# Optimization experiments

Measured on AMD Instinct MI355X. Metric: run time of the kernel, lower is better.

Reference implementation:

```python
import jax, jax.numpy as jnp
import numpy as np

K = 3
K2 = K * K
STRIDE, PAD, DIL = 1, 1, 1


def conv2d(x, w, b, stride, pad, dil):
    out = jax.lax.conv_general_dilated(
        x, w, (stride, stride), [(pad, pad), (pad, pad)],
        rhs_dilation=(dil, dil),
        dimension_numbers=("NCHW", "OIHW", "NCHW"))
    return out + b[None, :, None, None]


def deform_sample(img, py, px):
    """Bilinear sample with zero padding outside.
    img: [C,H,W]; py,px: [K2,Ho,Wo] float sample coords -> [C,K2,Ho,Wo]."""
    C, H, W = img.shape
    y0 = jnp.floor(py)
    x0 = jnp.floor(px)
    acc = jnp.zeros((C,) + py.shape, img.dtype)
    for dy in (0.0, 1.0):
        for dx in (0.0, 1.0):
            yi = y0 + dy
            xi = x0 + dx
            wgt = (1.0 - jnp.abs(py - yi)) * (1.0 - jnp.abs(px - xi))
            valid = (yi >= 0) & (yi < H) & (xi >= 0) & (xi < W)
            yc = jnp.clip(yi, 0, H - 1).astype(jnp.int32)
            xc = jnp.clip(xi, 0, W - 1).astype(jnp.int32)
            v = img[:, yc, xc]  # gather -> [C,K2,Ho,Wo]
            acc = acc + v * (wgt * valid)[None]
    return acc


def setup_inputs() -> dict:
    key = jax.random.key(0)
    k1, k2, k3, k4 = jax.random.split(key, 4)
    Cin, Cout = 64, 64
    x = jax.random.normal(k1, (4, Cin, 128, 128), jnp.float32)
    # small offset-conv weights so learned offsets stay in a few-pixel range
    w_off = jax.random.normal(k2, (3 * K2, Cin, K, K), jnp.float32) * 0.01
    b_off = jnp.zeros((3 * K2,), jnp.float32)
    # folded (BN-fused) deform conv weight/bias
    w = jax.random.normal(k3, (Cout, Cin, K, K), jnp.float32) * (1.0 / np.sqrt(Cin * K2))
    b = jax.random.normal(k4, (Cout,), jnp.float32) * 0.1
    return {"x": x, "w_off": w_off, "b_off": b_off, "w": w, "b": b}


def reference(x, w_off, b_off, w, b):
    N, C, H, W = x.shape
    # offset/mask conv -> chunk into (o1, o2, mask), cat offsets, sigmoid mask
    om = conv2d(x, w_off, b_off, STRIDE, PAD, DIL)  # [N, 27, Ho, Wo]
    o1, o2, m = jnp.split(om, 3, axis=1)
    offset = jnp.concatenate([o1, o2], axis=1)      # [N, 2*K2, Ho, Wo]
    mask = jax.nn.sigmoid(m)                        # [N, K2, Ho, Wo]
    Ho, Wo = offset.shape[2], offset.shape[3]
    # torchvision layout: per kernel tap (dy, dx) pairs
    off = offset.reshape(N, K2, 2, Ho, Wo)
    dy, dx = off[:, :, 0], off[:, :, 1]
    hk, wk = jnp.meshgrid(jnp.arange(K), jnp.arange(K), indexing="ij")
    base_y = ((jnp.arange(Ho) * STRIDE - PAD)[None, :, None]
              + (hk.reshape(K2) * DIL)[:, None, None])  # [K2,Ho,1]
    base_x = ((jnp.arange(Wo) * STRIDE - PAD)[None, None, :]
              + (wk.reshape(K2) * DIL)[:, None, None])  # [K2,1,Wo]
    py = base_y.astype(x.dtype) + dy                    # [N,K2,Ho,Wo]
    px = base_x.astype(x.dtype) + dx
    sampled = jax.vmap(deform_sample)(x, py, px)        # [N,C,K2,Ho,Wo]
    sampled = sampled * mask[:, None]
    out = jnp.einsum("ock,nckhw->nohw", w.reshape(w.shape[0], C, K2), sampled)
    out = out + b[None, :, None, None]
    return jax.nn.relu(out)
```

## Files before the change

kernel.cpp:

```cpp
#include <hip/hip_runtime.h>
#include <math.h>

#define N_ 4
#define C_ 64
#define H_ 128
#define W_ 128
#define HW_ (H_ * W_)
#define K2_ 9
#define COUT 64
#define CK 576
#define TP 16
#define SST 584

typedef __bf16 bf16x8 __attribute__((ext_vector_type(8)));
typedef __bf16 bf16x2 __attribute__((ext_vector_type(2)));
typedef float floatx4 __attribute__((ext_vector_type(4)));
typedef float floatx2 __attribute__((ext_vector_type(2)));

__device__ __forceinline__ float bflo(unsigned u) {
    return __builtin_bit_cast(float, u << 16);
}
__device__ __forceinline__ float bfhi(unsigned u) {
    return __builtin_bit_cast(float, u & 0xffff0000u);
}

__global__ __launch_bounds__(256) void prep_kernel(const float* __restrict__ x,
                                                   const float* __restrict__ w,
                                                   const float* __restrict__ w_off,
                                                   __bf16* __restrict__ xT,
                                                   __bf16* __restrict__ w2,
                                                   __bf16* __restrict__ w_off2) {
    __shared__ float s_t[64][33];
    int t = threadIdx.x;
    int bx = blockIdx.x;
    int y = blockIdx.y, n = blockIdx.z;
    if (bx < 4) {
        int x0 = bx * 32;
        int c = t >> 2, seg = (t & 3) * 8;
        const float* src = x + (((size_t)n * C_ + c) * H_ + y) * W_ + x0 + seg;
        floatx4 v0 = *(const floatx4*)src;
        floatx4 v1 = *(const floatx4*)(src + 4);
#pragma unroll
        for (int j = 0; j < 4; ++j) { s_t[c][seg + j] = v0[j]; s_t[c][seg + 4 + j] = v1[j]; }
        __syncthreads();
        int xl = t >> 3, cb = (t & 7) * 8;
        bf16x8 o;
#pragma unroll
        for (int j = 0; j < 8; ++j) o[j] = (__bf16)s_t[cb + j][xl];
        *(bf16x8*)(xT + (((size_t)n * H_ + y) * W_ + x0 + xl) * C_ + cb) = o;
    } else {
        int linear = (n * 128 + y) * 256 + t;
        if (linear < COUT * CK) {
            int o = linear / CK, r = linear - o * CK;
            int k = r >> 6, c = r & 63;
            w2[linear] = (__bf16)w[(o * C_ + c) * K2_ + k];
        }
        if (linear < 32 * CK) {
            int o = linear / CK, r = linear - o * CK;
            int k = r >> 6, c = r & 63;
            w_off2[linear] = (o < 27) ? (__bf16)w_off[(o * C_ + c) * K2_ + k] : (__bf16)0.f;
        }
    }
}

__device__ __forceinline__ floatx4 gemm_tile(const __bf16* __restrict__ arow,
                                             const __bf16* __restrict__ brow) {
    floatx4 acc = {0.f, 0.f, 0.f, 0.f};
#pragma unroll
    for (int it = 0; it < 18; ++it) {
        bf16x8 a  = *(const bf16x8*)(arow + 32 * it);
        bf16x8 bb = *(const bf16x8*)(brow + 32 * it);
        acc = __builtin_amdgcn_mfma_f32_16x16x32_bf16(a, bb, acc, 0, 0, 0);
    }
    return acc;
}

__global__ __launch_bounds__(256) void fused_kernel(const __bf16* __restrict__ xT,
                                                    const __bf16* __restrict__ w2,
                                                    const __bf16* __restrict__ w_off2,
                                                    const float* __restrict__ b_off,
                                                    const float* __restrict__ b,
                                                    float* __restrict__ out) {
    __shared__ __align__(16) __bf16 s_x[TP * SST];
    __shared__ float s_om[32 * TP];
    __shared__ floatx4 s_w4[K2_ * TP];
    __shared__ int s_pix[K2_ * TP];

    int t = threadIdx.x;
    int pixbase = blockIdx.x * TP;
    int wo0 = pixbase & (W_ - 1);
    int ho  = (pixbase >> 7) & (H_ - 1);
    int n   = pixbase >> 14;
    const __bf16* xn = xT + (size_t)n * HW_ * C_;

    int lane = t & 63;
    int wv   = t >> 6;
    int half = lane >> 5;
    int li   = lane & 31;

    {
        unsigned ua[18];
#pragma unroll
        for (int j = 0; j < 18; ++j) {
            int P = wv * 36 + 2 * j + half;
            int k = P >> 4, p = P & 15;
            int kh = k / 3, kw = k - kh * 3;
            int y  = ho - 1 + kh;
            int xx = wo0 + p - 1 + kw;
            int yc  = min(max(y, 0), H_ - 1);
            int xc2 = min(max(xx, 0), W_ - 1);
            unsigned pix = (unsigned)(yc * W_ + xc2);
            ua[j] = *(const unsigned*)(xn + (size_t)pix * C_ + 2 * li);
        }
#pragma unroll
        for (int j = 0; j < 18; ++j) {
            int P = wv * 36 + 2 * j + half;
            int k = P >> 4, p = P & 15;
            int kh = k / 3, kw = k - kh * 3;
            int y  = ho - 1 + kh;
            int xx = wo0 + p - 1 + kw;
            bool valid = ((unsigned)y < (unsigned)H_) && ((unsigned)xx < (unsigned)W_);
            unsigned v = valid ? ua[j] : 0u;
            *(unsigned*)&s_x[p * SST + k * 64 + 2 * li] = v;
        }
    }
    __syncthreads();

    int q   = lane >> 4;
    int col = lane & 15;
    const __bf16* brow = s_x + col * SST + q * 8;

    if (wv < 2) {
        int row = min(16 * wv + col, 26);
        floatx4 acc = gemm_tile(w_off2 + (size_t)row * CK + q * 8, brow);
#pragma unroll
        for (int r = 0; r < 4; ++r)
            s_om[(16 * wv + q * 4 + r) * TP + col] = acc[r];
    }
    __syncthreads();

    if (t < K2_ * TP) {
        int k  = t >> 4;
        int pp = t & 15;
        float dy = s_om[(2 * k) * TP + pp]     + b_off[2 * k];
        float dx = s_om[(2 * k + 1) * TP + pp] + b_off[2 * k + 1];
        float mm = s_om[(18 + k) * TP + pp]    + b_off[18 + k];
        float msk = 1.f / (1.f + expf(-mm));
        int kh = k / 3, kw = k - kh * 3;
        float py = (float)(ho - 1 + kh) + dy;
        float px = (float)(wo0 + pp - 1 + kw) + dx;
        float yf = floorf(py), xf = floorf(px);
        float fy = py - yf, fx = px - xf;
        int y0 = (int)yf, x0 = (int)xf;
        float wy0 = ((unsigned)y0 < (unsigned)H_)       ? 1.f - fy : 0.f;
        float wy1 = ((unsigned)(y0 + 1) < (unsigned)H_) ? fy       : 0.f;
        float wx0 = ((unsigned)x0 < (unsigned)W_)       ? 1.f - fx : 0.f;
        float wx1 = ((unsigned)(x0 + 1) < (unsigned)W_) ? fx       : 0.f;
        int y0c = min(max(y0, 0), H_ - 2);
        int x0c = min(max(x0, 0), W_ - 2);
        float t0 = (y0 == y0c) ? wy0 : ((y0 + 1 == y0c) ? wy1 : 0.f);
        float t1 = (y0 == y0c) ? wy1 : ((y0 == y0c + 1) ? wy0 : 0.f);
        float u0 = (x0 == x0c) ? wx0 : ((x0 + 1 == x0c) ? wx1 : 0.f);
        float u1 = (x0 == x0c) ? wx1 : ((x0 == x0c + 1) ? wx0 : 0.f);
        floatx4 w4 = { t0 * u0 * msk, t0 * u1 * msk, t1 * u0 * msk, t1 * u1 * msk };
        s_w4[t] = w4;
        s_pix[t] = y0c * W_ + x0c;
    }
    __syncthreads();

    {
        int Pb = wv * 36 + half;
        unsigned buf[3][4];
#pragma unroll
        for (int g = 0; g < 2; ++g) {
            int pix = s_pix[Pb + 2 * g];
            const unsigned* bp = (const unsigned*)(xn + (size_t)pix * C_) + li;
            buf[g][0] = bp[0];
            buf[g][1] = bp[32];
            buf[g][2] = bp[W_ * 32];
            buf[g][3] = bp[W_ * 32 + 32];
        }
#pragma unroll
        for (int g = 0; g < 18; ++g) {
            if (g < 16) {
                int pix = s_pix[Pb + 2 * (g + 2)];
                const unsigned* bp = (const unsigned*)(xn + (size_t)pix * C_) + li;
                unsigned* d = buf[(g + 2) % 3];
                d[0] = bp[0];
                d[1] = bp[32];
                d[2] = bp[W_ * 32];
                d[3] = bp[W_ * 32 + 32];
            }
            int P = Pb + 2 * g;
            floatx4 w4 = s_w4[P];
            const unsigned* a = buf[g % 3];
            float lo = w4[0] * bflo(a[0]) + w4[1] * bflo(a[1])
                     + w4[2] * bflo(a[2]) + w4[3] * bflo(a[3]);
            float hi = w4[0] * bfhi(a[0]) + w4[1] * bfhi(a[1])
                     + w4[2] * bfhi(a[2]) + w4[3] * bfhi(a[3]);
            floatx2 fv = {lo, hi};
            bf16x2 bv = __builtin_convertvector(fv, bf16x2);
            int k = P >> 4, p = P & 15;
            *(unsigned*)&s_x[p * SST + k * 64 + 2 * li] = __builtin_bit_cast(unsigned, bv);
        }
    }
    __syncthreads();

    {
        int row = 16 * wv + col;
        floatx4 acc = gemm_tile(w2 + (size_t)row * CK + q * 8, brow);
#pragma unroll
        for (int r = 0; r < 4; ++r) {
            int o = 16 * wv + q * 4 + r;
            float v = acc[r] + b[o];
            out[(((size_t)n * COUT + o) * H_ + ho) * W_ + wo0 + col] = fmaxf(v, 0.f);
        }
    }
}

extern "C" void kernel_launch(void* const* d_in, const int* in_sizes, int n_in,
                              void* d_out, int out_size, void* d_ws, size_t ws_size,
                              hipStream_t stream) {
    const float* x     = (const float*)d_in[0];
    const float* w_off = (const float*)d_in[1];
    const float* b_off = (const float*)d_in[2];
    const float* w     = (const float*)d_in[3];
    const float* b     = (const float*)d_in[4];
    float* out = (float*)d_out;

    __bf16* xT     = (__bf16*)d_ws;
    __bf16* w2     = xT + (size_t)N_ * HW_ * C_;
    __bf16* w_off2 = w2 + (size_t)COUT * CK;

    prep_kernel<<<dim3(5, 128, 4), 256, 0, stream>>>(x, w, w_off, xT, w2, w_off2);

    int nblocks = N_ * H_ * W_ / TP;
    fused_kernel<<<nblocks, 256, 0, stream>>>(xT, w2, w_off2, b_off, b, out);
}
```

Measured before the change: 136.8 us.

## Load offset-conv B operands directly from global and split K across four waves

The offset-conv stage no longer stages the 3x3 im2col patch into shared memory. Each of the four waves now loads its B operand straight from the transposed input in global memory and handles half of the reduction dimension for one 16-row block. The two K-halves are written to separate shared buffers and summed when the offsets are computed. This removes a shared-memory write pass and puts all four waves to work instead of two. The main GEMM also gets manual software prefetching of the A fragments. The risk is more uncoalesced global loads per lane and extra register pressure from the per-tap pixel indices.

```diff
diff --git a/kernel.cpp b/kernel.cpp
--- a/kernel.cpp
+++ b/kernel.cpp
@@ -63,18 +63,6 @@
     }
 }
 
-__device__ __forceinline__ floatx4 gemm_tile(const __bf16* __restrict__ arow,
-                                             const __bf16* __restrict__ brow) {
-    floatx4 acc = {0.f, 0.f, 0.f, 0.f};
-#pragma unroll
-    for (int it = 0; it < 18; ++it) {
-        bf16x8 a  = *(const bf16x8*)(arow + 32 * it);
-        bf16x8 bb = *(const bf16x8*)(brow + 32 * it);
-        acc = __builtin_amdgcn_mfma_f32_16x16x32_bf16(a, bb, acc, 0, 0, 0);
-    }
-    return acc;
-}
-
 __global__ __launch_bounds__(256) void fused_kernel(const __bf16* __restrict__ xT,
                                                     const __bf16* __restrict__ w2,
                                                     const __bf16* __restrict__ w_off2,
@@ -82,7 +70,7 @@
                                                     const float* __restrict__ b,
                                                     float* __restrict__ out) {
     __shared__ __align__(16) __bf16 s_x[TP * SST];
-    __shared__ float s_om[32 * TP];
+    __shared__ float s_om[2][32 * TP];
     __shared__ floatx4 s_w4[K2_ * TP];
     __shared__ int s_pix[K2_ * TP];
 
@@ -97,54 +85,50 @@
     int wv   = t >> 6;
     int half = lane >> 5;
     int li   = lane & 31;
+    int q    = lane >> 4;
+    int col  = lane & 15;
+
+    int  pixk[9];
+    bool vk[9];
+#pragma unroll
+    for (int k = 0; k < 9; ++k) {
+        int kh = k / 3, kw = k - kh * 3;
+        int y  = ho - 1 + kh;
+        int xx = wo0 + col - 1 + kw;
+        vk[k] = ((unsigned)y < (unsigned)H_) && ((unsigned)xx < (unsigned)W_);
+        int yc = min(max(y, 0), H_ - 1), xc = min(max(xx, 0), W_ - 1);
+        pixk[k] = yc * W_ + xc;
+    }
+    const bf16x8 bz = {(__bf16)0.f, (__bf16)0.f, (__bf16)0.f, (__bf16)0.f,
+                       (__bf16)0.f, (__bf16)0.f, (__bf16)0.f, (__bf16)0.f};
 
     {
-        unsigned ua[18];
-#pragma unroll
-        for (int j = 0; j < 18; ++j) {
-            int P = wv * 36 + 2 * j + half;
-            int k = P >> 4, p = P & 15;
-            int kh = k / 3, kw = k - kh * 3;
-            int y  = ho - 1 + kh;
-            int xx = wo0 + p - 1 + kw;
-            int yc  = min(max(y, 0), H_ - 1);
-            int xc2 = min(max(xx, 0), W_ - 1);
-            unsigned pix = (unsigned)(yc * W_ + xc2);
-            ua[j] = *(const unsigned*)(xn + (size_t)pix * C_ + 2 * li);
-        }
-#pragma unroll
-        for (int j = 0; j < 18; ++j) {
-            int P = wv * 36 + 2 * j + half;
-            int k = P >> 4, p = P & 15;
-            int kh = k / 3, kw = k - kh * 3;
-            int y  = ho - 1 + kh;
-            int xx = wo0 + p - 1 + kw;
-            bool valid = ((unsigned)y < (unsigned)H_) && ((unsigned)xx < (unsigned)W_);
-            unsigned v = valid ? ua[j] : 0u;
-            *(unsigned*)&s_x[p * SST + k * 64 + 2 * li] = v;
-        }
-    }
-    __syncthreads();
-
-    int q   = lane >> 4;
-    int col = lane & 15;
-    const __bf16* brow = s_x + col * SST + q * 8;
-
-    if (wv < 2) {
-        int row = min(16 * wv + col, 26);
-        floatx4 acc = gemm_tile(w_off2 + (size_t)row * CK + q * 8, brow);
-#pragma unroll
-        for (int r = 0; r < 4; ++r)
-            s_om[(16 * wv + q * 4 + r) * TP + col] = acc[r];
+        int h = wv & 1;
+        int r = wv >> 1;
+        const __bf16* ar = w_off2 + (size_t)(16 * r + col) * CK + h * 288 + q * 8;
+        floatx4 acc = {0.f, 0.f, 0.f, 0.f};
+#pragma unroll
+        for (int i = 0; i < 9; ++i) {
+            int ks  = h * 288 + 32 * i;
+            int tap = ks >> 6;
+            int cb  = ks & 63;
+            bf16x8 bb = *(const bf16x8*)(xn + (size_t)pixk[tap] * C_ + cb + q * 8);
+            bb = vk[tap] ? bb : bz;
+            bf16x8 a = *(const bf16x8*)(ar + 32 * i);
+            acc = __builtin_amdgcn_mfma_f32_16x16x32_bf16(a, bb, acc, 0, 0, 0);
+        }
+#pragma unroll
+        for (int rr = 0; rr < 4; ++rr)
+            s_om[h][(16 * r + q * 4 + rr) * TP + col] = acc[rr];
     }
     __syncthreads();
 
     if (t < K2_ * TP) {
         int k  = t >> 4;
         int pp = t & 15;
-        float dy = s_om[(2 * k) * TP + pp]     + b_off[2 * k];
-        float dx = s_om[(2 * k + 1) * TP + pp] + b_off[2 * k + 1];
-        float mm = s_om[(18 + k) * TP + pp]    + b_off[18 + k];
+        float dy = s_om[0][(2 * k) * TP + pp]     + s_om[1][(2 * k) * TP + pp]     + b_off[2 * k];
+        float dx = s_om[0][(2 * k + 1) * TP + pp] + s_om[1][(2 * k + 1) * TP + pp] + b_off[2 * k + 1];
+        float mm = s_om[0][(18 + k) * TP + pp]    + s_om[1][(18 + k) * TP + pp]    + b_off[18 + k];
         float msk = 1.f / (1.f + expf(-mm));
         int kh = k / 3, kw = k - kh * 3;
         float py = (float)(ho - 1 + kh) + dy;
@@ -207,8 +191,18 @@
     __syncthreads();
 
     {
-        int row = 16 * wv + col;
-        floatx4 acc = gemm_tile(w2 + (size_t)row * CK + q * 8, brow);
+        const __bf16* ar = w2 + (size_t)(16 * wv + col) * CK + q * 8;
+        const __bf16* brow = s_x + col * SST + q * 8;
+        floatx4 acc = {0.f, 0.f, 0.f, 0.f};
+        bf16x8 a_cur = *(const bf16x8*)ar;
+#pragma unroll
+        for (int it = 0; it < 18; ++it) {
+            bf16x8 a_nxt;
+            if (it < 17) a_nxt = *(const bf16x8*)(ar + 32 * (it + 1));
+            bf16x8 bb = *(const bf16x8*)(brow + 32 * it);
+            acc = __builtin_amdgcn_mfma_f32_16x16x32_bf16(a_cur, bb, acc, 0, 0, 0);
+            a_cur = a_nxt;
+        }
 #pragma unroll
         for (int r = 0; r < 4; ++r) {
             int o = 16 * wv + q * 4 + r;
```

After: 182.1 us. 1.33x slower.

## Process two 16-pixel tiles per block to reuse weight fragments across MFMAs

Applied to the files above, without the earlier changes.

Each block now handles 32 output pixels as two 16-pixel tiles, so every weight fragment loaded from global memory feeds two MFMAs. The offset-conv GEMM is split across all four waves by halving the K dimension, with the partial sums added in shared memory, and the main GEMM prefetches the next A fragment. This halves the block count and the per-pixel weight reloads, but doubles shared memory per block and register pressure (36-entry gather buffers), which may lower occupancy.

```diff
diff --git a/kernel.cpp b/kernel.cpp
--- a/kernel.cpp
+++ b/kernel.cpp
@@ -10,6 +10,7 @@
 #define COUT 64
 #define CK 576
 #define TP 16
+#define NT 2
 #define SST 584
 
 typedef __bf16 bf16x8 __attribute__((ext_vector_type(8)));
@@ -63,31 +64,19 @@
     }
 }
 
-__device__ __forceinline__ floatx4 gemm_tile(const __bf16* __restrict__ arow,
-                                             const __bf16* __restrict__ brow) {
-    floatx4 acc = {0.f, 0.f, 0.f, 0.f};
-#pragma unroll
-    for (int it = 0; it < 18; ++it) {
-        bf16x8 a  = *(const bf16x8*)(arow + 32 * it);
-        bf16x8 bb = *(const bf16x8*)(brow + 32 * it);
-        acc = __builtin_amdgcn_mfma_f32_16x16x32_bf16(a, bb, acc, 0, 0, 0);
-    }
-    return acc;
-}
-
 __global__ __launch_bounds__(256) void fused_kernel(const __bf16* __restrict__ xT,
                                                     const __bf16* __restrict__ w2,
                                                     const __bf16* __restrict__ w_off2,
                                                     const float* __restrict__ b_off,
                                                     const float* __restrict__ b,
                                                     float* __restrict__ out) {
-    __shared__ __align__(16) __bf16 s_x[TP * SST];
-    __shared__ float s_om[32 * TP];
-    __shared__ floatx4 s_w4[K2_ * TP];
-    __shared__ int s_pix[K2_ * TP];
+    __shared__ __align__(16) __bf16 s_x[NT][TP * SST];
+    __shared__ float s_om[NT][2][32 * TP];
+    __shared__ floatx4 s_w4[NT][K2_ * TP];
+    __shared__ int s_pix[NT][K2_ * TP];
 
     int t = threadIdx.x;
-    int pixbase = blockIdx.x * TP;
+    int pixbase = blockIdx.x * (TP * NT);
     int wo0 = pixbase & (W_ - 1);
     int ho  = (pixbase >> 7) & (H_ - 1);
     int n   = pixbase >> 14;
@@ -97,74 +86,94 @@
     int wv   = t >> 6;
     int half = lane >> 5;
     int li   = lane & 31;
-
-    {
-        unsigned ua[18];
-#pragma unroll
-        for (int j = 0; j < 18; ++j) {
-            int P = wv * 36 + 2 * j + half;
+    int q    = lane >> 4;
+    int col  = lane & 15;
+
+    {
+        unsigned ua[36];
+#pragma unroll
+        for (int j = 0; j < 36; ++j) {
+            int tl = j / 18, jj = j - 18 * tl;
+            int P = wv * 36 + 2 * jj + half;
             int k = P >> 4, p = P & 15;
             int kh = k / 3, kw = k - kh * 3;
             int y  = ho - 1 + kh;
-            int xx = wo0 + p - 1 + kw;
+            int xx = wo0 + 16 * tl + p - 1 + kw;
             int yc  = min(max(y, 0), H_ - 1);
             int xc2 = min(max(xx, 0), W_ - 1);
             unsigned pix = (unsigned)(yc * W_ + xc2);
             ua[j] = *(const unsigned*)(xn + (size_t)pix * C_ + 2 * li);
         }
 #pragma unroll
-        for (int j = 0; j < 18; ++j) {
-            int P = wv * 36 + 2 * j + half;
+        for (int j = 0; j < 36; ++j) {
+            int tl = j / 18, jj = j - 18 * tl;
+            int P = wv * 36 + 2 * jj + half;
             int k = P >> 4, p = P & 15;
             int kh = k / 3, kw = k - kh * 3;
             int y  = ho - 1 + kh;
-            int xx = wo0 + p - 1 + kw;
+            int xx = wo0 + 16 * tl + p - 1 + kw;
             bool valid = ((unsigned)y < (unsigned)H_) && ((unsigned)xx < (unsigned)W_);
             unsigned v = valid ? ua[j] : 0u;
-            *(unsigned*)&s_x[p * SST + k * 64 + 2 * li] = v;
-        }
-    }
-    __syncthreads();
-
-    int q   = lane >> 4;
-    int col = lane & 15;
-    const __bf16* brow = s_x + col * SST + q * 8;
-
-    if (wv < 2) {
-        int row = min(16 * wv + col, 26);
-        floatx4 acc = gemm_tile(w_off2 + (size_t)row * CK + q * 8, brow);
-#pragma unroll
-        for (int r = 0; r < 4; ++r)
-            s_om[(16 * wv + q * 4 + r) * TP + col] = acc[r];
-    }
-    __syncthreads();
-
-    if (t < K2_ * TP) {
-        int k  = t >> 4;
-        int pp = t & 15;
-        float dy = s_om[(2 * k) * TP + pp]     + b_off[2 * k];
-        float dx = s_om[(2 * k + 1) * TP + pp] + b_off[2 * k + 1];
-        float mm = s_om[(18 + k) * TP + pp]    + b_off[18 + k];
-        float msk = 1.f / (1.f + expf(-mm));
-        int kh = k / 3, kw = k - kh * 3;
-        float py = (float)(ho - 1 + kh) + dy;
-        float px = (float)(wo0 + pp - 1 + kw) + dx;
-        float yf = floorf(py), xf = floorf(px);
-        float fy = py - yf, fx = px - xf;
-        int y0 = (int)yf, x0 = (int)xf;
-        float wy0 = ((unsigned)y0 < (unsigned)H_)       ? 1.f - fy : 0.f;
-        float wy1 = ((unsigned)(y0 + 1) < (unsigned)H_) ? fy       : 0.f;
-        float wx0 = ((unsigned)x0 < (unsigned)W_)       ? 1.f - fx : 0.f;
-        float wx1 = ((unsigned)(x0 + 1) < (unsigned)W_) ? fx       : 0.f;
-        int y0c = min(max(y0, 0), H_ - 2);
-        int x0c = min(max(x0, 0), W_ - 2);
-        float t0 = (y0 == y0c) ? wy0 : ((y0 + 1 == y0c) ? wy1 : 0.f);
-        float t1 = (y0 == y0c) ? wy1 : ((y0 == y0c + 1) ? wy0 : 0.f);
-        float u0 = (x0 == x0c) ? wx0 : ((x0 + 1 == x0c) ? wx1 : 0.f);
-        float u1 = (x0 == x0c) ? wx1 : ((x0 == x0c + 1) ? wx0 : 0.f);
-        floatx4 w4 = { t0 * u0 * msk, t0 * u1 * msk, t1 * u0 * msk, t1 * u1 * msk };
-        s_w4[t] = w4;
-        s_pix[t] = y0c * W_ + x0c;
+            *(unsigned*)&s_x[tl][p * SST + k * 64 + 2 * li] = v;
+        }
+    }
+    __syncthreads();
+
+    {
+        int r = wv >> 1;
+        int h = wv & 1;
+        const __bf16* ar = w_off2 + (size_t)(16 * r + col) * CK + h * 288 + q * 8;
+        const __bf16* b0 = s_x[0] + col * SST + h * 288 + q * 8;
+        const __bf16* b1 = s_x[1] + col * SST + h * 288 + q * 8;
+        floatx4 acc0 = {0.f, 0.f, 0.f, 0.f}, acc1 = {0.f, 0.f, 0.f, 0.f};
+#pragma unroll
+        for (int it = 0; it < 9; ++it) {
+            bf16x8 a   = *(const bf16x8*)(ar + 32 * it);
+            bf16x8 bb0 = *(const bf16x8*)(b0 + 32 * it);
+            bf16x8 bb1 = *(const bf16x8*)(b1 + 32 * it);
+            acc0 = __builtin_amdgcn_mfma_f32_16x16x32_bf16(a, bb0, acc0, 0, 0, 0);
+            acc1 = __builtin_amdgcn_mfma_f32_16x16x32_bf16(a, bb1, acc1, 0, 0, 0);
+        }
+#pragma unroll
+        for (int rr = 0; rr < 4; ++rr) {
+            s_om[0][h][(16 * r + q * 4 + rr) * TP + col] = acc0[rr];
+            s_om[1][h][(16 * r + q * 4 + rr) * TP + col] = acc1[rr];
+        }
+    }
+    __syncthreads();
+
+#pragma unroll
+    for (int it2 = 0; it2 < 2; ++it2) {
+        int i = it2 * 256 + t;
+        if (i < NT * K2_ * TP) {
+            int tl = (i >= 144);
+            int P  = i - 144 * tl;
+            int k  = P >> 4;
+            int pp = P & 15;
+            float dy = s_om[tl][0][(2 * k) * TP + pp]     + s_om[tl][1][(2 * k) * TP + pp]     + b_off[2 * k];
+            float dx = s_om[tl][0][(2 * k + 1) * TP + pp] + s_om[tl][1][(2 * k + 1) * TP + pp] + b_off[2 * k + 1];
+            float mm = s_om[tl][0][(18 + k) * TP + pp]    + s_om[tl][1][(18 + k) * TP + pp]    + b_off[18 + k];
+            float msk = 1.f / (1.f + expf(-mm));
+            int kh = k / 3, kw = k - kh * 3;
+            float py = (float)(ho - 1 + kh) + dy;
+            float px = (float)(wo0 + 16 * tl + pp - 1 + kw) + dx;
+            float yf = floorf(py), xf = floorf(px);
+            float fy = py - yf, fx = px - xf;
+            int y0 = (int)yf, x0 = (int)xf;
+            float wy0 = ((unsigned)y0 < (unsigned)H_)       ? 1.f - fy : 0.f;
+            float wy1 = ((unsigned)(y0 + 1) < (unsigned)H_) ? fy       : 0.f;
+            float wx0 = ((unsigned)x0 < (unsigned)W_)       ? 1.f - fx : 0.f;
+            float wx1 = ((unsigned)(x0 + 1) < (unsigned)W_) ? fx       : 0.f;
+            int y0c = min(max(y0, 0), H_ - 2);
+            int x0c = min(max(x0, 0), W_ - 2);
+            float t0 = (y0 == y0c) ? wy0 : ((y0 + 1 == y0c) ? wy1 : 0.f);
+            float t1 = (y0 == y0c) ? wy1 : ((y0 == y0c + 1) ? wy0 : 0.f);
+            float u0 = (x0 == x0c) ? wx0 : ((x0 + 1 == x0c) ? wx1 : 0.f);
+            float u1 = (x0 == x0c) ? wx1 : ((x0 == x0c + 1) ? wx0 : 0.f);
+            floatx4 w4 = { t0 * u0 * msk, t0 * u1 * msk, t1 * u0 * msk, t1 * u1 * msk };
+            s_w4[tl][P] = w4;
+            s_pix[tl][P] = y0c * W_ + x0c;
+        }
     }
     __syncthreads();
 
@@ -173,7 +182,7 @@
         unsigned buf[3][4];
 #pragma unroll
         for (int g = 0; g < 2; ++g) {
-            int pix = s_pix[Pb + 2 * g];
+            int pix = s_pix[0][Pb + 2 * g];
             const unsigned* bp = (const unsigned*)(xn + (size_t)pix * C_) + li;
             buf[g][0] = bp[0];
             buf[g][1] = bp[32];
@@ -181,18 +190,21 @@
             buf[g][3] = bp[W_ * 32 + 32];
         }
 #pragma unroll
-        for (int g = 0; g < 18; ++g) {
-            if (g < 16) {
-                int pix = s_pix[Pb + 2 * (g + 2)];
+        for (int g = 0; g < 36; ++g) {
+            if (g < 34) {
+                int gn = g + 2;
+                int tln = (gn >= 18);
+                int pix = s_pix[tln][Pb + 2 * (gn - 18 * tln)];
                 const unsigned* bp = (const unsigned*)(xn + (size_t)pix * C_) + li;
-                unsigned* d = buf[(g + 2) % 3];
+                unsigned* d = buf[gn % 3];
                 d[0] = bp[0];
                 d[1] = bp[32];
                 d[2] = bp[W_ * 32];
                 d[3] = bp[W_ * 32 + 32];
             }
-            int P = Pb + 2 * g;
-            floatx4 w4 = s_w4[P];
+            int tl = (g >= 18);
+            int P = Pb + 2 * (g - 18 * tl);
+            floatx4 w4 = s_w4[tl][P];
             const unsigned* a = buf[g % 3];
             float lo = w4[0] * bflo(a[0]) + w4[1] * bflo(a[1])
                      + w4[2] * bflo(a[2]) + w4[3] * bflo(a[3]);
@@ -201,19 +213,34 @@
             floatx2 fv = {lo, hi};
             bf16x2 bv = __builtin_convertvector(fv, bf16x2);
             int k = P >> 4, p = P & 15;
-            *(unsigned*)&s_x[p * SST + k * 64 + 2 * li] = __builtin_bit_cast(unsigned, bv);
-        }
-    }
-    __syncthreads();
-
-    {
-        int row = 16 * wv + col;
-        floatx4 acc = gemm_tile(w2 + (size_t)row * CK + q * 8, brow);
+            *(unsigned*)&s_x[tl][p * SST + k * 64 + 2 * li] = __builtin_bit_cast(unsigned, bv);
+        }
+    }
+    __syncthreads();
+
+    {
+        const __bf16* ar = w2 + (size_t)(16 * wv + col) * CK + q * 8;
+        const __bf16* b0 = s_x[0] + col * SST + q * 8;
+        const __bf16* b1 = s_x[1] + col * SST + q * 8;
+        floatx4 acc0 = {0.f, 0.f, 0.f, 0.f}, acc1 = {0.f, 0.f, 0.f, 0.f};
+        bf16x8 a_cur = *(const bf16x8*)ar;
+#pragma unroll
+        for (int it = 0; it < 18; ++it) {
+            bf16x8 a_nxt;
+            if (it < 17) a_nxt = *(const bf16x8*)(ar + 32 * (it + 1));
+            bf16x8 bb0 = *(const bf16x8*)(b0 + 32 * it);
+            bf16x8 bb1 = *(const bf16x8*)(b1 + 32 * it);
+            acc0 = __builtin_amdgcn_mfma_f32_16x16x32_bf16(a_cur, bb0, acc0, 0, 0, 0);
+            acc1 = __builtin_amdgcn_mfma_f32_16x16x32_bf16(a_cur, bb1, acc1, 0, 0, 0);
+            a_cur = a_nxt;
+        }
 #pragma unroll
         for (int r = 0; r < 4; ++r) {
             int o = 16 * wv + q * 4 + r;
-            float v = acc[r] + b[o];
-            out[(((size_t)n * COUT + o) * H_ + ho) * W_ + wo0 + col] = fmaxf(v, 0.f);
+            float bias = b[o];
+            float* ob = out + (((size_t)n * COUT + o) * H_ + ho) * W_ + wo0;
+            ob[col]      = fmaxf(acc0[r] + bias, 0.f);
+            ob[16 + col] = fmaxf(acc1[r] + bias, 0.f);
         }
     }
 }
@@ -234,6 +261,6 @@
 
     prep_kernel<<<dim3(5, 128, 4), 256, 0, stream>>>(x, w, w_off, xT, w2, w_off2);
 
-    int nblocks = N_ * H_ * W_ / TP;
+    int nblocks = N_ * H_ * W_ / (TP * NT);
     fused_kernel<<<nblocks, 256, 0, stream>>>(xT, w2, w_off2, b_off, b, out);
 }
```

After: 123.9 us. 9.4% less time.

## Process two pixel tiles per 512-thread block and split offset GEMM over K

Applied to the files above, without the earlier changes.

Each block now handles two 16-pixel tiles with 512 threads, so all eight waves take part in the offset-conv GEMM by splitting its K dimension in half and summing partials in shared memory. Before, only two of four waves did that GEMM. The main GEMM software-prefetches the next weight fragment from global memory. The cost is doubled shared memory per block and a larger block size, which may lower occupancy.

```diff
diff --git a/kernel.cpp b/kernel.cpp
--- a/kernel.cpp
+++ b/kernel.cpp
@@ -10,6 +10,7 @@
 #define COUT 64
 #define CK 576
 #define TP 16
+#define NT 2
 #define SST 584
 
 typedef __bf16 bf16x8 __attribute__((ext_vector_type(8)));
@@ -63,31 +64,19 @@
     }
 }
 
-__device__ __forceinline__ floatx4 gemm_tile(const __bf16* __restrict__ arow,
-                                             const __bf16* __restrict__ brow) {
-    floatx4 acc = {0.f, 0.f, 0.f, 0.f};
-#pragma unroll
-    for (int it = 0; it < 18; ++it) {
-        bf16x8 a  = *(const bf16x8*)(arow + 32 * it);
-        bf16x8 bb = *(const bf16x8*)(brow + 32 * it);
-        acc = __builtin_amdgcn_mfma_f32_16x16x32_bf16(a, bb, acc, 0, 0, 0);
-    }
-    return acc;
-}
-
-__global__ __launch_bounds__(256) void fused_kernel(const __bf16* __restrict__ xT,
+__global__ __launch_bounds__(512) void fused_kernel(const __bf16* __restrict__ xT,
                                                     const __bf16* __restrict__ w2,
                                                     const __bf16* __restrict__ w_off2,
                                                     const float* __restrict__ b_off,
                                                     const float* __restrict__ b,
                                                     float* __restrict__ out) {
-    __shared__ __align__(16) __bf16 s_x[TP * SST];
-    __shared__ float s_om[32 * TP];
-    __shared__ floatx4 s_w4[K2_ * TP];
-    __shared__ int s_pix[K2_ * TP];
+    __shared__ __align__(16) __bf16 s_x[NT][TP * SST];
+    __shared__ float s_om[NT][2][32 * TP];
+    __shared__ floatx4 s_w4[NT][K2_ * TP];
+    __shared__ int s_pix[NT][K2_ * TP];
 
     int t = threadIdx.x;
-    int pixbase = blockIdx.x * TP;
+    int pixbase = blockIdx.x * (TP * NT);
     int wo0 = pixbase & (W_ - 1);
     int ho  = (pixbase >> 7) & (H_ - 1);
     int n   = pixbase >> 14;
@@ -97,16 +86,20 @@
     int wv   = t >> 6;
     int half = lane >> 5;
     int li   = lane & 31;
+    int q    = lane >> 4;
+    int col  = lane & 15;
+    int tl   = wv >> 2;
+    int w4i  = wv & 3;
 
     {
         unsigned ua[18];
 #pragma unroll
         for (int j = 0; j < 18; ++j) {
-            int P = wv * 36 + 2 * j + half;
+            int P = w4i * 36 + 2 * j + half;
             int k = P >> 4, p = P & 15;
             int kh = k / 3, kw = k - kh * 3;
             int y  = ho - 1 + kh;
-            int xx = wo0 + p - 1 + kw;
+            int xx = wo0 + 16 * tl + p - 1 + kw;
             int yc  = min(max(y, 0), H_ - 1);
             int xc2 = min(max(xx, 0), W_ - 1);
             unsigned pix = (unsigned)(yc * W_ + xc2);
@@ -114,41 +107,49 @@
         }
 #pragma unroll
         for (int j = 0; j < 18; ++j) {
-            int P = wv * 36 + 2 * j + half;
+            int P = w4i * 36 + 2 * j + half;
             int k = P >> 4, p = P & 15;
             int kh = k / 3, kw = k - kh * 3;
             int y  = ho - 1 + kh;
-            int xx = wo0 + p - 1 + kw;
+            int xx = wo0 + 16 * tl + p - 1 + kw;
             bool valid = ((unsigned)y < (unsigned)H_) && ((unsigned)xx < (unsigned)W_);
             unsigned v = valid ? ua[j] : 0u;
-            *(unsigned*)&s_x[p * SST + k * 64 + 2 * li] = v;
-        }
-    }
-    __syncthreads();
-
-    int q   = lane >> 4;
-    int col = lane & 15;
-    const __bf16* brow = s_x + col * SST + q * 8;
-
-    if (wv < 2) {
-        int row = min(16 * wv + col, 26);
-        floatx4 acc = gemm_tile(w_off2 + (size_t)row * CK + q * 8, brow);
-#pragma unroll
-        for (int r = 0; r < 4; ++r)
-            s_om[(16 * wv + q * 4 + r) * TP + col] = acc[r];
-    }
-    __syncthreads();
-
-    if (t < K2_ * TP) {
-        int k  = t >> 4;
-        int pp = t & 15;
-        float dy = s_om[(2 * k) * TP + pp]     + b_off[2 * k];
-        float dx = s_om[(2 * k + 1) * TP + pp] + b_off[2 * k + 1];
-        float mm = s_om[(18 + k) * TP + pp]    + b_off[18 + k];
+            *(unsigned*)&s_x[tl][p * SST + k * 64 + 2 * li] = v;
+        }
+    }
+    __syncthreads();
+
+    {
+        int btl = wv >> 2;
+        int r   = (wv >> 1) & 1;
+        int h   = wv & 1;
+        const __bf16* ar = w_off2 + (size_t)(16 * r + col) * CK + h * 288 + q * 8;
+        const __bf16* bb = s_x[btl] + col * SST + h * 288 + q * 8;
+        floatx4 acc = {0.f, 0.f, 0.f, 0.f};
+#pragma unroll
+        for (int it = 0; it < 9; ++it) {
+            bf16x8 a  = *(const bf16x8*)(ar + 32 * it);
+            bf16x8 bv = *(const bf16x8*)(bb + 32 * it);
+            acc = __builtin_amdgcn_mfma_f32_16x16x32_bf16(a, bv, acc, 0, 0, 0);
+        }
+#pragma unroll
+        for (int rr = 0; rr < 4; ++rr)
+            s_om[btl][h][(16 * r + q * 4 + rr) * TP + col] = acc[rr];
+    }
+    __syncthreads();
+
+    if (t < NT * K2_ * TP) {
+        int ctl = (t >= 144);
+        int P   = t - 144 * ctl;
+        int k   = P >> 4;
+        int pp  = P & 15;
+        float dy = s_om[ctl][0][(2 * k) * TP + pp]     + s_om[ctl][1][(2 * k) * TP + pp]     + b_off[2 * k];
+        float dx = s_om[ctl][0][(2 * k + 1) * TP + pp] + s_om[ctl][1][(2 * k + 1) * TP + pp] + b_off[2 * k + 1];
+        float mm = s_om[ctl][0][(18 + k) * TP + pp]    + s_om[ctl][1][(18 + k) * TP + pp]    + b_off[18 + k];
         float msk = 1.f / (1.f + expf(-mm));
         int kh = k / 3, kw = k - kh * 3;
         float py = (float)(ho - 1 + kh) + dy;
-        float px = (float)(wo0 + pp - 1 + kw) + dx;
+        float px = (float)(wo0 + 16 * ctl + pp - 1 + kw) + dx;
         float yf = floorf(py), xf = floorf(px);
         float fy = py - yf, fx = px - xf;
         int y0 = (int)yf, x0 = (int)xf;
@@ -163,17 +164,17 @@
         float u0 = (x0 == x0c) ? wx0 : ((x0 + 1 == x0c) ? wx1 : 0.f);
         float u1 = (x0 == x0c) ? wx1 : ((x0 == x0c + 1) ? wx0 : 0.f);
         floatx4 w4 = { t0 * u0 * msk, t0 * u1 * msk, t1 * u0 * msk, t1 * u1 * msk };
-        s_w4[t] = w4;
-        s_pix[t] = y0c * W_ + x0c;
-    }
-    __syncthreads();
-
-    {
-        int Pb = wv * 36 + half;
+        s_w4[ctl][P] = w4;
+        s_pix[ctl][P] = y0c * W_ + x0c;
+    }
+    __syncthreads();
+
+    {
+        int Pb = w4i * 36 + half;
         unsigned buf[3][4];
 #pragma unroll
         for (int g = 0; g < 2; ++g) {
-            int pix = s_pix[Pb + 2 * g];
+            int pix = s_pix[tl][Pb + 2 * g];
             const unsigned* bp = (const unsigned*)(xn + (size_t)pix * C_) + li;
             buf[g][0] = bp[0];
             buf[g][1] = bp[32];
@@ -183,7 +184,7 @@
 #pragma unroll
         for (int g = 0; g < 18; ++g) {
             if (g < 16) {
-                int pix = s_pix[Pb + 2 * (g + 2)];
+                int pix = s_pix[tl][Pb + 2 * (g + 2)];
                 const unsigned* bp = (const unsigned*)(xn + (size_t)pix * C_) + li;
                 unsigned* d = buf[(g + 2) % 3];
                 d[0] = bp[0];
@@ -192,7 +193,7 @@
                 d[3] = bp[W_ * 32 + 32];
             }
             int P = Pb + 2 * g;
-            floatx4 w4 = s_w4[P];
+            floatx4 w4 = s_w4[tl][P];
             const unsigned* a = buf[g % 3];
             float lo = w4[0] * bflo(a[0]) + w4[1] * bflo(a[1])
                      + w4[2] * bflo(a[2]) + w4[3] * bflo(a[3]);
@@ -201,19 +202,30 @@
             floatx2 fv = {lo, hi};
             bf16x2 bv = __builtin_convertvector(fv, bf16x2);
             int k = P >> 4, p = P & 15;
-            *(unsigned*)&s_x[p * SST + k * 64 + 2 * li] = __builtin_bit_cast(unsigned, bv);
-        }
-    }
-    __syncthreads();
-
-    {
-        int row = 16 * wv + col;
-        floatx4 acc = gemm_tile(w2 + (size_t)row * CK + q * 8, brow);
+            *(unsigned*)&s_x[tl][p * SST + k * 64 + 2 * li] = __builtin_bit_cast(unsigned, bv);
+        }
+    }
+    __syncthreads();
+
+    {
+        int ot = w4i;
+        const __bf16* ar = w2 + (size_t)(16 * ot + col) * CK + q * 8;
+        const __bf16* bb = s_x[tl] + col * SST + q * 8;
+        floatx4 acc = {0.f, 0.f, 0.f, 0.f};
+        bf16x8 a_cur = *(const bf16x8*)ar;
+#pragma unroll
+        for (int it = 0; it < 18; ++it) {
+            bf16x8 a_nxt;
+            if (it < 17) a_nxt = *(const bf16x8*)(ar + 32 * (it + 1));
+            bf16x8 bv = *(const bf16x8*)(bb + 32 * it);
+            acc = __builtin_amdgcn_mfma_f32_16x16x32_bf16(a_cur, bv, acc, 0, 0, 0);
+            a_cur = a_nxt;
+        }
 #pragma unroll
         for (int r = 0; r < 4; ++r) {
-            int o = 16 * wv + q * 4 + r;
+            int o = 16 * ot + q * 4 + r;
             float v = acc[r] + b[o];
-            out[(((size_t)n * COUT + o) * H_ + ho) * W_ + wo0 + col] = fmaxf(v, 0.f);
+            out[(((size_t)n * COUT + o) * H_ + ho) * W_ + wo0 + 16 * tl + col] = fmaxf(v, 0.f);
         }
     }
 }
@@ -234,6 +246,6 @@
 
     prep_kernel<<<dim3(5, 128, 4), 256, 0, stream>>>(x, w, w_off, xT, w2, w_off2);
 
-    int nblocks = N_ * H_ * W_ / TP;
-    fused_kernel<<<nblocks, 256, 0, stream>>>(xT, w2, w_off2, b_off, b, out);
-}
+    int nblocks = N_ * H_ * W_ / (TP * NT);
+    fused_kernel<<<nblocks, 512, 0, stream>>>(xT, w2, w_off2, b_off, b, out);
+}
```

Result: slower. 145.3 us (+6.2%).
